# Optimization experiments

Hardware: AMD Instinct MI355X
Metric: run time of the kernel (lower is better)

Reference implementation:

```python
import jax, jax.numpy as jnp
import numpy as np
from jax import lax

B, S, T = 4096, 512, 25


def setup_inputs() -> dict:
    key = jax.random.key(0)
    k1, k2, k3, k4, k5, k6 = jax.random.split(key, 6)
    emissions = jax.random.normal(k1, (B, S, T), dtype=jnp.float32)
    start_transitions = jax.random.normal(k2, (T,), dtype=jnp.float32) * 0.1
    end_transitions = jax.random.normal(k3, (T,), dtype=jnp.float32) * 0.1
    transitions = jax.random.normal(k4, (T, T), dtype=jnp.float32) * 0.1
    labels = jax.random.randint(k5, (B, S), 0, T, dtype=jnp.int32)
    lengths = jax.random.randint(k6, (B,), S // 2, S + 1, dtype=jnp.int32)
    mask = jnp.arange(S, dtype=jnp.int32)[None, :] < lengths[:, None]  # [B,S] bool, mask[:,0]=True
    return {"emissions": emissions, "start_transitions": start_transitions,
            "end_transitions": end_transitions, "transitions": transitions,
            "labels": labels, "mask": mask}


def _crf_llh(emissions, start_transitions, end_transitions, transitions, labels, mask):
    # torchcrf.CRF forward with batch_first=True, reduction='token_mean'
    b, s, t = emissions.shape
    maskf = mask.astype(emissions.dtype)

    # ---- numerator: score of the gold tag sequence ----
    first_tags = labels[:, 0]                                  # [B]
    score = start_transitions[first_tags] + emissions[jnp.arange(b), 0, first_tags]
    trans_scores = transitions[labels[:, :-1], labels[:, 1:]]  # [B,S-1]
    emit_scores = jnp.take_along_axis(emissions, labels[..., None], axis=2)[..., 0]  # [B,S]
    score = score + jnp.sum((trans_scores + emit_scores[:, 1:]) * maskf[:, 1:], axis=1)
    seq_lens = jnp.sum(mask.astype(jnp.int32), axis=1)         # [B]
    last_tags = jnp.take_along_axis(labels, (seq_lens - 1)[:, None], axis=1)[:, 0]
    numerator = score + end_transitions[last_tags]

    # ---- denominator: forward algorithm (log partition) ----
    alpha0 = start_transitions[None, :] + emissions[:, 0]      # [B,T]

    def step(alpha, xs):
        emit_t, mask_t = xs                                    # [B,T], [B]
        # broadcast: alpha[b,i] + transitions[i,j] + emit_t[b,j]
        next_alpha = jax.nn.logsumexp(alpha[:, :, None] + transitions[None, :, :]
                                      + emit_t[:, None, :], axis=1)
        alpha = jnp.where(mask_t[:, None], next_alpha, alpha)
        return alpha, None

    emits = jnp.swapaxes(emissions[:, 1:], 0, 1)               # [S-1,B,T]
    masks = jnp.swapaxes(mask[:, 1:], 0, 1)                    # [S-1,B]
    alpha, _ = lax.scan(step, alpha0, (emits, masks))
    denominator = jax.nn.logsumexp(alpha + end_transitions[None, :], axis=1)  # [B]

    llh = numerator - denominator                              # [B]
    return jnp.sum(llh) / jnp.sum(maskf)                       # token_mean


def reference(emissions, start_transitions, end_transitions, transitions, labels, mask):
    return _crf_llh(emissions, start_transitions, end_transitions, transitions, labels, mask)
```

## Files before the change

### kernel.cpp

```cpp
#include <hip/hip_runtime.h>
#include <stdint.h>

#define TT 25
#define SS 512
#define BB 4096
#define RST 36
#define IL2 1.4426950408889634f
#define LN2F 0.6931471805599453f

__device__ __forceinline__ float ex2(float x){ return __builtin_amdgcn_exp2f(x); }
__device__ __forceinline__ float lg2(float x){ return __builtin_amdgcn_logf(x); }

#define PIN(x) asm volatile("" : "+v"(x))

template<int K>
__device__ __forceinline__ float rotk(float v){
  if constexpr (K == 0) return v;
  else return __int_as_float(__builtin_amdgcn_update_dpp(
      0, __float_as_int(v), 0x120 | K, 0xF, 0xF, true));
}

#define SWZMAX(v,P) v = fmaxf(v, __int_as_float(__builtin_amdgcn_ds_swizzle(__float_as_int(v), P)))
#define SWZADD(v,P) v += __int_as_float(__builtin_amdgcn_ds_swizzle(__float_as_int(v), P))

__device__ __forceinline__ int mask_at(const void* m, int mode, int idx){
  if (mode == 1) return ((const int*)m)[idx] != 0;
  if (mode == 2) return ((const float*)m)[idx] != 0.0f;
  return ((const unsigned char*)m)[idx] != 0;
}

__global__ __launch_bounds__(256, 2)
void crf_main(const float* __restrict__ em, const float* __restrict__ startp,
              const float* __restrict__ endp, const float* __restrict__ transp,
              const int* __restrict__ labels, const void* __restrict__ maskp,
              float* __restrict__ wsr, float* __restrict__ wsl)
{
  __shared__ float smem[16 * RST];
  const int tid  = threadIdx.x;
  const int w    = tid >> 6;
  const int lane = tid & 63;
  const int g    = lane >> 4;
  const int lidx = lane & 15;
  const int dir  = g & 1;
  const int rsel = g >> 1;
  const int row  = blockIdx.x * 8 + w * 2 + rsel;
  const int rowbase = (w * 4 + g) * RST;

  const int c1 = 2 * lidx, c2 = 2 * lidx + 1;
  const bool v1 = (c1 < TT), v2 = (c2 < TT);
  const int c1c = v1 ? c1 : (TT - 1), c2c = v2 ? c2 : (TT - 1);
  const int cb  = (lidx < 12) ? c1 : 23;
  const bool selA = (lidx < 12);
  const int ws2 = (lidx <= 12) ? 2 * lidx : (26 + 2 * (lidx - 13));

  const int emW  = row * (SS * TT);
  const int labW = row * SS;

  const uint32_t w0 = ((const uint32_t*)maskp)[0];
  const int mode = (w0 == 1u) ? 1 : ((w0 == 0x3F800000u) ? 2 : 0);

  int lens[2];
  const int base2row = blockIdx.x * 8 + w * 2;
#pragma unroll
  for (int r = 0; r < 2; ++r) {
    int mb = (base2row + r) * SS;
    int pq1 = mask_at(maskp, mode, mb + lane * 8);
    unsigned long long b1 = __ballot(pq1);
    int q = __popcll(b1);
    int bs = 8 * (q - 1);
    int pq2 = mask_at(maskp, mode, mb + bs + (lane & 7));
    unsigned long long b2 = __ballot((lane < 8) && pq2);
    lens[r] = bs + __popcll(b2);
  }
  const int L = rsel ? lens[1] : lens[0];
  const int m = (L - 1) >> 1;
  const int iters = dir ? (L - 1 - m) : m;
  const int it0 = lens[0] - 1 - ((lens[0] - 1) >> 1);
  const int it1 = lens[1] - 1 - ((lens[1] - 1) >> 1);
  const int maxIters = max(it0, it1);

  float Ea1[16], Eb1[16], Ea2[16], Eb2[16];
#pragma unroll
  for (int k = 0; k < 16; ++k) {
    int s  = (lidx - k) & 15;
    int i1 = 2 * s, i2 = 2 * s + 1;
    bool q1 = (i1 < TT), q2 = (i2 < TT);
    int i1c = q1 ? i1 : 0, i2c = q2 ? i2 : 0;
    float t11 = dir ? transp[c1c * TT + i1c] : transp[i1c * TT + c1c];
    float t21 = dir ? transp[c1c * TT + i2c] : transp[i2c * TT + c1c];
    float t12 = dir ? transp[c2c * TT + i1c] : transp[i1c * TT + c2c];
    float t22 = dir ? transp[c2c * TT + i2c] : transp[i2c * TT + c2c];
    Ea1[k] = (q1 && v1) ? ex2(t11 * IL2) : 0.f;
    Eb1[k] = (q2 && v1) ? ex2(t21 * IL2) : 0.f;
    Ea2[k] = (q1 && v2) ? ex2(t12 * IL2) : 0.f;
    Eb2[k] = (q2 && v2) ? ex2(t22 * IL2) : 0.f;
  }
#pragma unroll
  for (int k = 0; k < 16; ++k) {
    PIN(Ea1[k]); PIN(Eb1[k]); PIN(Ea2[k]); PIN(Eb2[k]);
  }

  float pf1 = startp[c1c] + em[emW + c1c];
  float pf2 = startp[c2c] + em[emW + c2c];
  float p1 = v1 ? ex2((dir ? endp[c1c] : pf1) * IL2) : 0.f;
  float p2 = v2 ? ex2((dir ? endp[c2c] : pf2) * IL2) : 0.f;

  const int l0 = labels[labW];
  const int lE = labels[labW + L - 1];
  float num = dir ? endp[lE] : (startp[l0] + em[emW + l0]);
  int C2 = 0;
  int carry = dir ? lE : l0;

  float emp1[4], emp2[4], tv[4], eg[4];
  int labv[4];
#pragma unroll
  for (int u = 0; u < 4; ++u) {
    int t  = dir ? (L - 1 - u) : (1 + u);
    int o  = emW + t * TT + cb;
    emp1[u] = em[o];
    emp2[u] = em[o + 1];
    int ni = dir ? (L - 2 - u) : (1 + u);
    int nl = labels[labW + ni];
    int aL = dir ? nl : carry, bL = dir ? carry : nl;
    tv[u] = transp[aL * TT + bL];
    eg[u] = em[emW + t * TT + bL];
    carry = nl;
    labv[u] = labels[labW + (dir ? (L - 6 - u) : (5 + u))];
  }

  int emOff  = emW + (dir ? (L - 5) * TT : 5 * TT) + cb;
  int labOff = labW + (dir ? (L - 10) : 9);
  const int dstep = dir ? -TT : TT;
  const int dlab  = dir ? -1 : 1;

  int ubase = 0;

#define ROTK(K)                                                               \
    { float r1 = rotk<K>(w1), r2 = rotk<K>(w2v);                              \
      d1a = fmaf(r1, Ea1[K], d1a); d1b = fmaf(r2, Eb1[K], d1b);               \
      d2a = fmaf(r1, Ea2[K], d2a); d2b = fmaf(r2, Eb2[K], d2b); }

#define STEP(u, FILL)                                                         \
  {                                                                           \
    bool live = (ubase + (u)) < iters;                                        \
    float ev1 = selA ? emp1[u] : emp2[u];                                     \
    float ev2 = emp2[u];                                                      \
    float e1 = ex2(ev1 * IL2), e2 = ex2(ev2 * IL2);                           \
    float ta = tv[u] + eg[u];                                                 \
    num += live ? ta : 0.f;                                                   \
    if (FILL) {                                                               \
      emp1[u] = em[emOff];                                                    \
      emp2[u] = em[emOff + 1];                                                \
      int nl = labv[u];                                                       \
      int aL = dir ? nl : carry, bL = dir ? carry : nl;                       \
      tv[u] = transp[aL * TT + bL];                                           \
      int ego = max(emOff + bL - cb, emW);                                    \
      eg[u] = em[ego];                                                        \
      labv[u] = labels[labOff];                                               \
      carry = nl;                                                             \
      emOff  = max(emOff + dstep, emW);                                       \
      labOff = max(labOff + dlab, labW);                                      \
    }                                                                         \
    float w1 = dir ? p1 * e1 : p1, w2v = dir ? p2 * e2 : p2;                  \
    float d1a = 0.f, d1b = 0.f, d2a = 0.f, d2b = 0.f;                         \
    ROTK(0)  ROTK(1)  ROTK(2)  ROTK(3)                                        \
    ROTK(4)  ROTK(5)  ROTK(6)  ROTK(7)                                        \
    ROTK(8)  ROTK(9)  ROTK(10) ROTK(11)                                       \
    ROTK(12) ROTK(13) ROTK(14) ROTK(15)                                       \
    float d1 = d1a + d1b, d2 = d2a + d2b;                                     \
    float p1n = dir ? d1 : d1 * e1, p2n = dir ? d2 : d2 * e2;                 \
    p1 = live ? p1n : p1; p2 = live ? p2n : p2;                               \
  }

#define RESCALE {                                                             \
    float mx = fmaxf(p1, p2);                                                 \
    SWZMAX(mx, 0x041F); SWZMAX(mx, 0x081F);                                   \
    SWZMAX(mx, 0x101F); SWZMAX(mx, 0x201F);                                   \
    int ef = (__float_as_int(mx) >> 23) & 0xFF;                               \
    C2 += ef - 127;                                                           \
    float sc = __int_as_float((254 - ef) << 23);                              \
    p1 *= sc; p2 *= sc; }

  for (; ubase + 8 <= maxIters; ubase += 8) {
    STEP(0, 1) STEP(1, 1) STEP(2, 1) STEP(3, 1)
    STEP(0, 1) STEP(1, 1) STEP(2, 1) STEP(3, 1)
    RESCALE
  }
  {
    int rem = maxIters - ubase;
    if (rem > 0) STEP(0, 1)
    if (rem > 1) STEP(1, 1)
    if (rem > 2) STEP(2, 1)
    if (rem > 3) STEP(3, 1)
    if (rem > 4) STEP(0, 0)
    if (rem > 5) STEP(1, 0)
    if (rem > 6) STEP(2, 0)
  }
  RESCALE

#undef STEP
#undef ROTK
#undef RESCALE

  ((float2*)smem)[(rowbase + ws2) >> 1] = make_float2(p1, p2);
  smem[rowbase + 32] = num;
  smem[rowbase + 33] = __int_as_float(C2);
  const int pbase = (w * 4 + (g ^ 1)) * RST;
  float2 qq = ((float2*)smem)[(pbase + ws2) >> 1];
  float prod = p1 * qq.x + p2 * qq.y;
  SWZADD(prod, 0x041F); SWZADD(prod, 0x081F);
  SWZADD(prod, 0x101F); SWZADD(prod, 0x201F);
  float onum = smem[pbase + 32];
  int oC2 = __float_as_int(smem[pbase + 33]);
  if (lidx == 0 && dir == 0) {
    float den = LN2F * (lg2(prod) + (float)(C2 + oC2));
    wsr[row] = (num + onum) - den;
    wsl[row] = (float)L;
  }
}

__global__ void crf_reduce(const float* __restrict__ wsr,
                           const float* __restrict__ wsl,
                           float* __restrict__ out)
{
  __shared__ float sr[256], sl[256];
  int t = threadIdx.x;
  float a = 0.0f, c = 0.0f;
  for (int i = t; i < BB; i += 256) { a += wsr[i]; c += wsl[i]; }
  sr[t] = a; sl[t] = c;
  __syncthreads();
  for (int k = 128; k > 0; k >>= 1) {
    if (t < k) { sr[t] += sr[t + k]; sl[t] += sl[t + k]; }
    __syncthreads();
  }
  if (t == 0) out[0] = sr[0] / sl[0];
}

extern "C" void kernel_launch(void* const* d_in, const int* in_sizes, int n_in,
                              void* d_out, int out_size, void* d_ws, size_t ws_size,
                              hipStream_t stream)
{
  const float* em = (const float*)d_in[0];
  const float* st = (const float*)d_in[1];
  const float* en = (const float*)d_in[2];
  const float* tr = (const float*)d_in[3];
  const int*   lb = (const int*)d_in[4];
  const void*  mk = d_in[5];
  float* wsr = (float*)d_ws;
  float* wsl = wsr + BB;
  crf_main<<<BB / 8, 256, 0, stream>>>(em, st, en, tr, lb, mk, wsr, wsl);
  crf_reduce<<<1, 256, 0, stream>>>(wsr, wsl, (float*)d_out);
}
```

Before: 122.3 us.

## Use packed FP32 FMA for forward recursion and peel liveness checks

Repacks the transition weights into float2 pairs and runs the 16-lane rotate-accumulate through v_pk_fma_f32 with op_sel, halving the FMA instruction count per step. It also adds a first loop up to the shorter row's iteration count that skips the per-step liveness selects. Inline asm can limit the compiler's scheduling, and packed FMA needs the DPP-rotated values placed in adjacent registers, which may add moves.

```diff
diff --git a/kernel.cpp b/kernel.cpp
--- a/kernel.cpp
+++ b/kernel.cpp
@@ -8,6 +8,8 @@
 #define IL2 1.4426950408889634f
 #define LN2F 0.6931471805599453f
 
+typedef float v2f __attribute__((ext_vector_type(2)));
+
 __device__ __forceinline__ float ex2(float x){ return __builtin_amdgcn_exp2f(x); }
 __device__ __forceinline__ float lg2(float x){ return __builtin_amdgcn_logf(x); }
 
@@ -18,6 +20,21 @@
   if constexpr (K == 0) return v;
   else return __int_as_float(__builtin_amdgcn_update_dpp(
       0, __float_as_int(v), 0x120 | K, 0xF, 0xF, true));
+}
+
+__device__ __forceinline__ void pkfma_lo(v2f &d, v2f r, v2f w){
+  asm("v_pk_fma_f32 %0, %1, %2, %0 op_sel:[0,0,0] op_sel_hi:[0,1,1]"
+      : "+v"(d) : "v"(r), "v"(w));
+}
+__device__ __forceinline__ void pkfma_hi(v2f &d, v2f r, v2f w){
+  asm("v_pk_fma_f32 %0, %1, %2, %0 op_sel:[1,0,0] op_sel_hi:[1,1,1]"
+      : "+v"(d) : "v"(r), "v"(w));
+}
+__device__ __forceinline__ v2f pkmul(v2f a, v2f b){
+  v2f d; asm("v_pk_mul_f32 %0, %1, %2" : "=v"(d) : "v"(a), "v"(b)); return d;
+}
+__device__ __forceinline__ v2f pkadd(v2f a, v2f b){
+  v2f d; asm("v_pk_add_f32 %0, %1, %2" : "=v"(d) : "v"(a), "v"(b)); return d;
 }
 
 #define SWZMAX(v,P) v = fmaxf(v, __int_as_float(__builtin_amdgcn_ds_swizzle(__float_as_int(v), P)))
@@ -78,8 +95,9 @@
   const int it0 = lens[0] - 1 - ((lens[0] - 1) >> 1);
   const int it1 = lens[1] - 1 - ((lens[1] - 1) >> 1);
   const int maxIters = max(it0, it1);
-
-  float Ea1[16], Eb1[16], Ea2[16], Eb2[16];
+  const int minIters = min((lens[0] - 1) >> 1, (lens[1] - 1) >> 1);
+
+  v2f Wt[32];
 #pragma unroll
   for (int k = 0; k < 16; ++k) {
     int s  = (lidx - k) & 15;
@@ -90,20 +108,19 @@
     float t21 = dir ? transp[c1c * TT + i2c] : transp[i2c * TT + c1c];
     float t12 = dir ? transp[c2c * TT + i1c] : transp[i1c * TT + c2c];
     float t22 = dir ? transp[c2c * TT + i2c] : transp[i2c * TT + c2c];
-    Ea1[k] = (q1 && v1) ? ex2(t11 * IL2) : 0.f;
-    Eb1[k] = (q2 && v1) ? ex2(t21 * IL2) : 0.f;
-    Ea2[k] = (q1 && v2) ? ex2(t12 * IL2) : 0.f;
-    Eb2[k] = (q2 && v2) ? ex2(t22 * IL2) : 0.f;
-  }
-#pragma unroll
-  for (int k = 0; k < 16; ++k) {
-    PIN(Ea1[k]); PIN(Eb1[k]); PIN(Ea2[k]); PIN(Eb2[k]);
-  }
+    Wt[2*k].x   = (q1 && v1) ? ex2(t11 * IL2) : 0.f;
+    Wt[2*k].y   = (q1 && v2) ? ex2(t12 * IL2) : 0.f;
+    Wt[2*k+1].x = (q2 && v1) ? ex2(t21 * IL2) : 0.f;
+    Wt[2*k+1].y = (q2 && v2) ? ex2(t22 * IL2) : 0.f;
+  }
+#pragma unroll
+  for (int k = 0; k < 32; ++k) PIN(Wt[k]);
 
   float pf1 = startp[c1c] + em[emW + c1c];
   float pf2 = startp[c2c] + em[emW + c2c];
-  float p1 = v1 ? ex2((dir ? endp[c1c] : pf1) * IL2) : 0.f;
-  float p2 = v2 ? ex2((dir ? endp[c2c] : pf2) * IL2) : 0.f;
+  v2f P;
+  P.x = v1 ? ex2((dir ? endp[c1c] : pf1) * IL2) : 0.f;
+  P.y = v2 ? ex2((dir ? endp[c2c] : pf2) * IL2) : 0.f;
 
   const int l0 = labels[labW];
   const int lE = labels[labW + L - 1];
@@ -135,19 +152,19 @@
 
   int ubase = 0;
 
-#define ROTK(K)                                                               \
-    { float r1 = rotk<K>(w1), r2 = rotk<K>(w2v);                              \
-      d1a = fmaf(r1, Ea1[K], d1a); d1b = fmaf(r2, Eb1[K], d1b);               \
-      d2a = fmaf(r1, Ea2[K], d2a); d2b = fmaf(r2, Eb2[K], d2b); }
-
-#define STEP(u, FILL)                                                         \
+#define RK(K, D)                                                              \
+    { v2f R; R.x = rotk<K>(Wv.x); R.y = rotk<K>(Wv.y);                        \
+      pkfma_lo(D, R, Wt[2*(K)]);                                              \
+      pkfma_hi(D, R, Wt[2*(K)+1]); }
+
+#define STEP(u, FILL, LIVE)                                                   \
   {                                                                           \
-    bool live = (ubase + (u)) < iters;                                        \
     float ev1 = selA ? emp1[u] : emp2[u];                                     \
-    float ev2 = emp2[u];                                                      \
-    float e1 = ex2(ev1 * IL2), e2 = ex2(ev2 * IL2);                           \
+    v2f E; E.x = ex2(ev1 * IL2); E.y = ex2(emp2[u] * IL2);                    \
     float ta = tv[u] + eg[u];                                                 \
-    num += live ? ta : 0.f;                                                   \
+    bool live = true;                                                         \
+    if (LIVE) { live = (ubase + (u)) < iters; num += live ? ta : 0.f; }       \
+    else num += ta;                                                           \
     if (FILL) {                                                               \
       emp1[u] = em[emOff];                                                    \
       emp2[u] = em[emOff + 1];                                                \
@@ -161,53 +178,59 @@
       emOff  = max(emOff + dstep, emW);                                       \
       labOff = max(labOff + dlab, labW);                                      \
     }                                                                         \
-    float w1 = dir ? p1 * e1 : p1, w2v = dir ? p2 * e2 : p2;                  \
-    float d1a = 0.f, d1b = 0.f, d2a = 0.f, d2b = 0.f;                         \
-    ROTK(0)  ROTK(1)  ROTK(2)  ROTK(3)                                        \
-    ROTK(4)  ROTK(5)  ROTK(6)  ROTK(7)                                        \
-    ROTK(8)  ROTK(9)  ROTK(10) ROTK(11)                                       \
-    ROTK(12) ROTK(13) ROTK(14) ROTK(15)                                       \
-    float d1 = d1a + d1b, d2 = d2a + d2b;                                     \
-    float p1n = dir ? d1 : d1 * e1, p2n = dir ? d2 : d2 * e2;                 \
-    p1 = live ? p1n : p1; p2 = live ? p2n : p2;                               \
+    v2f Wv = dir ? pkmul(P, E) : P;                                           \
+    v2f D0 = {0.f,0.f}, D1 = {0.f,0.f}, D2 = {0.f,0.f}, D3 = {0.f,0.f};       \
+    RK(0, D0)  RK(1, D1)  RK(2, D2)  RK(3, D3)                                \
+    RK(4, D0)  RK(5, D1)  RK(6, D2)  RK(7, D3)                                \
+    RK(8, D0)  RK(9, D1)  RK(10,D2)  RK(11,D3)                                \
+    RK(12,D0)  RK(13,D1)  RK(14,D2)  RK(15,D3)                                \
+    D0 = pkadd(D0, D1); D2 = pkadd(D2, D3); D0 = pkadd(D0, D2);               \
+    v2f Pn = dir ? D0 : pkmul(D0, E);                                         \
+    if (LIVE) { P.x = live ? Pn.x : P.x; P.y = live ? Pn.y : P.y; }           \
+    else P = Pn;                                                              \
   }
 
 #define RESCALE {                                                             \
-    float mx = fmaxf(p1, p2);                                                 \
+    float mx = fmaxf(P.x, P.y);                                               \
     SWZMAX(mx, 0x041F); SWZMAX(mx, 0x081F);                                   \
     SWZMAX(mx, 0x101F); SWZMAX(mx, 0x201F);                                   \
     int ef = (__float_as_int(mx) >> 23) & 0xFF;                               \
     C2 += ef - 127;                                                           \
     float sc = __int_as_float((254 - ef) << 23);                              \
-    p1 *= sc; p2 *= sc; }
-
+    P.x *= sc; P.y *= sc; }
+
+  for (; ubase + 8 <= minIters; ubase += 8) {
+    STEP(0, 1, 0) STEP(1, 1, 0) STEP(2, 1, 0) STEP(3, 1, 0)
+    STEP(0, 1, 0) STEP(1, 1, 0) STEP(2, 1, 0) STEP(3, 1, 0)
+    RESCALE
+  }
   for (; ubase + 8 <= maxIters; ubase += 8) {
-    STEP(0, 1) STEP(1, 1) STEP(2, 1) STEP(3, 1)
-    STEP(0, 1) STEP(1, 1) STEP(2, 1) STEP(3, 1)
+    STEP(0, 1, 1) STEP(1, 1, 1) STEP(2, 1, 1) STEP(3, 1, 1)
+    STEP(0, 1, 1) STEP(1, 1, 1) STEP(2, 1, 1) STEP(3, 1, 1)
     RESCALE
   }
   {
     int rem = maxIters - ubase;
-    if (rem > 0) STEP(0, 1)
-    if (rem > 1) STEP(1, 1)
-    if (rem > 2) STEP(2, 1)
-    if (rem > 3) STEP(3, 1)
-    if (rem > 4) STEP(0, 0)
-    if (rem > 5) STEP(1, 0)
-    if (rem > 6) STEP(2, 0)
+    if (rem > 0) STEP(0, 1, 1)
+    if (rem > 1) STEP(1, 1, 1)
+    if (rem > 2) STEP(2, 1, 1)
+    if (rem > 3) STEP(3, 1, 1)
+    if (rem > 4) STEP(0, 0, 1)
+    if (rem > 5) STEP(1, 0, 1)
+    if (rem > 6) STEP(2, 0, 1)
   }
   RESCALE
 
 #undef STEP
-#undef ROTK
+#undef RK
 #undef RESCALE
 
-  ((float2*)smem)[(rowbase + ws2) >> 1] = make_float2(p1, p2);
+  ((float2*)smem)[(rowbase + ws2) >> 1] = make_float2(P.x, P.y);
   smem[rowbase + 32] = num;
   smem[rowbase + 33] = __int_as_float(C2);
   const int pbase = (w * 4 + (g ^ 1)) * RST;
   float2 qq = ((float2*)smem)[(pbase + ws2) >> 1];
-  float prod = p1 * qq.x + p2 * qq.y;
+  float prod = P.x * qq.x + P.y * qq.y;
   SWZADD(prod, 0x041F); SWZADD(prod, 0x081F);
   SWZADD(prod, 0x101F); SWZADD(prod, 0x201F);
   float onum = smem[pbase + 32];
```

Result: no change. 124.1 us (+1.5%).
